# Kernel tuning notes

Hardware: AMD Instinct MI355X
Metric: run time of the kernel (lower is better)

Reference implementation:

```python
import jax, jax.numpy as jnp
import numpy as np

N_NODES = 50000
N_EDGES = 800000
BATCH = 4


def setup_inputs() -> dict:
    key = jax.random.key(0)
    ks = jax.random.split(key, 12)
    inp = {
        "x": jax.random.normal(ks[0], (BATCH, N_NODES, 1, 1), dtype=jnp.float32),
        "edge_index": jax.random.randint(ks[1], (2, N_EDGES), 0, N_NODES, dtype=jnp.int64),
        "W_conv1": jax.random.normal(ks[2], (3, 1, 32), dtype=jnp.float32) * 0.1,
        "b_conv1": jnp.zeros((3, 32), dtype=jnp.float32),
        "W_lin1": jax.random.normal(ks[3], (3, 64, 32), dtype=jnp.float32) * 0.1,
        "b_lin1": jnp.zeros((3, 32), dtype=jnp.float32),
        "att1": jax.random.uniform(ks[4], (1,), dtype=jnp.float32),
        "W_conv2": jax.random.normal(ks[5], (3, 32, 32), dtype=jnp.float32) * 0.1,
        "b_conv2": jnp.zeros((3, 32), dtype=jnp.float32),
        "W_lin2": jax.random.normal(ks[6], (3, 64, 32), dtype=jnp.float32) * 0.1,
        "b_lin2": jnp.zeros((3, 32), dtype=jnp.float32),
        "att2": jax.random.uniform(ks[7], (1,), dtype=jnp.float32),
        "W_out": jax.random.normal(ks[8], (32, 1), dtype=jnp.float32) * 0.1,
        "b_out": jnp.zeros((1,), dtype=jnp.float32),
    }
    return inp


def _gcn(h, W, b, src, dst, norm, inv_deg, n):
    # h: (B,N,Fin) -> (B,N,Fout); symmetric-normalized GCNConv with self loops
    xw = h @ W                                   # (B,N,Fout)
    msg = xw[:, src, :] * norm[None, :, None]    # (B,E,Fout)
    agg = jax.ops.segment_sum(jnp.swapaxes(msg, 0, 1), dst, num_segments=n)
    agg = jnp.swapaxes(agg, 0, 1)                # (B,N,Fout)
    return agg + xw * inv_deg[None, :, None] + b


def _tgcn_cell(h_in, Wc, bc, Wl, bl, att, src, dst, norm, inv_deg, n):
    # TGCN2 GRU cell with H0 = 0, weighted by softmax(att) (periods=1 -> weight 1)
    B = h_in.shape[0]
    out_dim = Wc.shape[-1]
    H = jnp.zeros((B, n, out_dim), dtype=h_in.dtype)
    cz = _gcn(h_in, Wc[0], bc[0], src, dst, norm, inv_deg, n)
    Z = jax.nn.sigmoid(jnp.concatenate([cz, H], axis=-1) @ Wl[0] + bl[0])
    cr = _gcn(h_in, Wc[1], bc[1], src, dst, norm, inv_deg, n)
    R = jax.nn.sigmoid(jnp.concatenate([cr, H], axis=-1) @ Wl[1] + bl[1])
    ch = _gcn(h_in, Wc[2], bc[2], src, dst, norm, inv_deg, n)
    Ht = jnp.tanh(jnp.concatenate([ch, H * R], axis=-1) @ Wl[2] + bl[2])
    Hn = Z * H + (1.0 - Z) * Ht
    a = jax.nn.softmax(att)  # (1,) -> [1.0]
    return a[0] * Hn


def reference(x, edge_index, W_conv1, b_conv1, W_lin1, b_lin1, att1,
              W_conv2, b_conv2, W_lin2, b_lin2, att2, W_out, b_out):
    n = x.shape[1]
    src, dst = edge_index[0], edge_index[1]
    ones = jnp.ones(src.shape[0], dtype=x.dtype)
    deg = jax.ops.segment_sum(ones, dst, num_segments=n) + 1.0  # + self loop
    dis = jax.lax.rsqrt(deg)
    norm = dis[src] * dis[dst]   # (E,)
    inv_deg = 1.0 / deg          # self-loop norm

    h = x[..., 0]  # (B,N,1) periods=1
    h = jax.nn.relu(_tgcn_cell(h, W_conv1, b_conv1, W_lin1, b_lin1, att1,
                               src, dst, norm, inv_deg, n))
    h = jax.nn.relu(_tgcn_cell(h, W_conv2, b_conv2, W_lin2, b_lin2, att2,
                               src, dst, norm, inv_deg, n))
    return h @ W_out + b_out  # (B,N,1)
```

## Files before the change

kernel.cpp:

```cpp
#include <hip/hip_runtime.h>
#include <hip/hip_fp16.h>
#include <stdint.h>

#define N_NODES 50000
#define BATCH 4
#define CAP 64

__global__ void fill_kernel(const int* __restrict__ src,
                            const int* __restrict__ dst,
                            int* __restrict__ cursor,
                            unsigned short* __restrict__ bucket, int E) {
    int e = blockIdx.x * blockDim.x + threadIdx.x;
    if (e < E) {
        int d = dst[e];
        int pos = atomicAdd(&cursor[d], 1);
        if (pos < CAP) bucket[d * CAP + pos] = (unsigned short)src[e];
    }
}

__global__ void dis_xd_kernel(const int* __restrict__ deg,
                              const float* __restrict__ x,
                              float* __restrict__ dis,
                              float4* __restrict__ xd, int N) {
    int n = blockIdx.x * blockDim.x + threadIdx.x;
    if (n >= N) return;
    float d = rsqrtf((float)(deg[n] + 1));
    dis[n] = d;
    xd[n] = make_float4(x[n] * d, x[N + n] * d, x[2 * N + n] * d,
                        x[3 * N + n] * d);
}

__global__ void precomp_kernel(const float* __restrict__ Wc1,
                               const float* __restrict__ bc1,
                               const float* __restrict__ Wl1,
                               const float* __restrict__ bl1,
                               const float* __restrict__ Wc2,
                               const float* __restrict__ bc2,
                               const float* __restrict__ Wl2,
                               const float* __restrict__ bl2,
                               float* __restrict__ pc) {
    int i = blockIdx.x * blockDim.x + threadIdx.x;
    if (i < 2048) {
        int g = i >> 10;
        int kf = i & 1023;
        int k = kf >> 5, f = kf & 31;
        int gate = g ? 2 : 0;
        float s = 0.0f;
        for (int j = 0; j < 32; ++j)
            s += Wc2[gate * 1024 + k * 32 + j] * Wl2[gate * 2048 + j * 32 + f];
        pc[i] = s;
    } else if (i < 2112) {
        int g = (i - 2048) >> 5;
        int f = i & 31;
        int gate = g ? 2 : 0;
        float s = bl2[gate * 32 + f];
        for (int j = 0; j < 32; ++j)
            s += bc2[gate * 32 + j] * Wl2[gate * 2048 + j * 32 + f];
        pc[i] = s;
    } else if (i < 2240) {
        int t = i - 2112;
        int which = t >> 5;
        int f = t & 31;
        int gate = (which >= 2) ? 2 : 0;
        if ((which & 1) == 0) {
            float s = 0.0f;
            for (int j = 0; j < 32; ++j)
                s += Wc1[gate * 32 + j] * Wl1[gate * 2048 + j * 32 + f];
            pc[i] = s;
        } else {
            float s = bl1[gate * 32 + f];
            for (int j = 0; j < 32; ++j)
                s += bc1[gate * 32 + j] * Wl1[gate * 2048 + j * 32 + f];
            pc[i] = s;
        }
    }
}

__global__ void s1h1_kernel(const float4* __restrict__ xd,
                            const float* __restrict__ dis,
                            const int* __restrict__ deg,
                            const unsigned short* __restrict__ bucket,
                            const float* __restrict__ pc,
                            char* __restrict__ hs, int N) {
    int idx = blockIdx.x * blockDim.x + threadIdx.x;
    int node = idx >> 3;
    if (node >= N) return;
    int j = idx & 7;
    int cnt = deg[node];
    if (cnt > CAP) cnt = CAP;
    float ax, ay, az, aw;
    if (j == 0) {
        float4 v = xd[node];
        ax = v.x; ay = v.y; az = v.z; aw = v.w;
    } else {
        ax = ay = az = aw = 0.f;
    }
    for (int i = j; i < cnt; i += 8) {
        int s = bucket[node * CAP + i];
        float4 v = xd[s];
        ax += v.x; ay += v.y; az += v.z; aw += v.w;
    }
#pragma unroll
    for (int m = 4; m; m >>= 1) {
        ax += __shfl_xor(ax, m, 64);
        ay += __shfl_xor(ay, m, 64);
        az += __shfl_xor(az, m, 64);
        aw += __shfl_xor(aw, m, 64);
    }
    float d = dis[node];
    float t0 = ax * d, t1 = ay * d, t2 = az * d, t3 = aw * d;
#pragma unroll
    for (int m = 0; m < 4; ++m) {
        int f = j + 8 * m;
        float uz = pc[2112 + f], vz = pc[2144 + f];
        float uh = pc[2176 + f], vh = pc[2208 + f];
        float h0 = fmaxf((1.0f - 1.0f / (1.0f + expf(-(t0 * uz + vz)))) *
                         tanhf(t0 * uh + vh), 0.0f) * d;
        float h1 = fmaxf((1.0f - 1.0f / (1.0f + expf(-(t1 * uz + vz)))) *
                         tanhf(t1 * uh + vh), 0.0f) * d;
        float h2 = fmaxf((1.0f - 1.0f / (1.0f + expf(-(t2 * uz + vz)))) *
                         tanhf(t2 * uh + vh), 0.0f) * d;
        float h3 = fmaxf((1.0f - 1.0f / (1.0f + expf(-(t3 * uz + vz)))) *
                         tanhf(t3 * uh + vh), 0.0f) * d;
        __half2 lo = __floats2half2_rn(h0, h1);
        __half2 hi = __floats2half2_rn(h2, h3);
        uint2 u;
        u.x = *reinterpret_cast<unsigned int*>(&lo);
        u.y = *reinterpret_cast<unsigned int*>(&hi);
        *reinterpret_cast<uint2*>(hs + (size_t)node * 256 + f * 8) = u;
    }
}

__global__ __launch_bounds__(256) void l2_agg_kernel(
    const char* __restrict__ hs, const float* __restrict__ dis,
    const int* __restrict__ deg, const unsigned short* __restrict__ bucket,
    const float* __restrict__ pc, const float* __restrict__ Wout,
    const float* __restrict__ bout, float* __restrict__ out, int N) {
    int lane = threadIdx.x & 63;
    int f = lane & 31;
    int h = lane >> 5;

    float mcol[32];
#pragma unroll
    for (int k = 0; k < 32; ++k) mcol[k] = pc[h * 1024 + k * 32 + f];
    float wv = pc[2048 + h * 32 + f];
    float wf = Wout[f];
    float bo = bout[0];
    const char* hp = hs + f * 8 + h * 4;

    int wid = (blockIdx.x * blockDim.x + threadIdx.x) >> 6;
    int nw = (gridDim.x * blockDim.x) >> 6;

    for (int node = wid; node < N; node += nw) {
        int cnt = deg[node];
        if (cnt > CAP) cnt = CAP;
        unsigned int bidx = bucket[node * CAP + lane];
        __half2 sv = *(const __half2*)(hp + (size_t)node * 256);
        float2 fs = __half22float2(sv);
        float accx = fs.x, accy = fs.y;
        int i = 0;
        for (; i + 8 <= cnt; i += 8) {
            unsigned int o0 = __builtin_amdgcn_readlane(bidx, i) * 256u;
            unsigned int o1 = __builtin_amdgcn_readlane(bidx, i + 1) * 256u;
            unsigned int o2 = __builtin_amdgcn_readlane(bidx, i + 2) * 256u;
            unsigned int o3 = __builtin_amdgcn_readlane(bidx, i + 3) * 256u;
            unsigned int o4 = __builtin_amdgcn_readlane(bidx, i + 4) * 256u;
            unsigned int o5 = __builtin_amdgcn_readlane(bidx, i + 5) * 256u;
            unsigned int o6 = __builtin_amdgcn_readlane(bidx, i + 6) * 256u;
            unsigned int o7 = __builtin_amdgcn_readlane(bidx, i + 7) * 256u;
            __half2 v0 = *(const __half2*)(hp + o0);
            __half2 v1 = *(const __half2*)(hp + o1);
            __half2 v2 = *(const __half2*)(hp + o2);
            __half2 v3 = *(const __half2*)(hp + o3);
            __half2 v4 = *(const __half2*)(hp + o4);
            __half2 v5 = *(const __half2*)(hp + o5);
            __half2 v6 = *(const __half2*)(hp + o6);
            __half2 v7 = *(const __half2*)(hp + o7);
            float2 f0 = __half22float2(v0), f1 = __half22float2(v1);
            float2 f2 = __half22float2(v2), f3 = __half22float2(v3);
            float2 f4 = __half22float2(v4), f5 = __half22float2(v5);
            float2 f6 = __half22float2(v6), f7 = __half22float2(v7);
            accx += ((f0.x + f1.x) + (f2.x + f3.x)) +
                    ((f4.x + f5.x) + (f6.x + f7.x));
            accy += ((f0.y + f1.y) + (f2.y + f3.y)) +
                    ((f4.y + f5.y) + (f6.y + f7.y));
        }
        for (; i < cnt; ++i) {
            unsigned int o = __builtin_amdgcn_readlane(bidx, i) * 256u;
            float2 fv = __half22float2(*(const __half2*)(hp + o));
            accx += fv.x;
            accy += fv.y;
        }

        float g0 = 0.f, g1 = 0.f, g2 = 0.f, g3 = 0.f;
#pragma unroll
        for (int k = 0; k < 32; ++k) {
            float tb0 = __int_as_float(
                __builtin_amdgcn_readlane(__float_as_int(accx), k));
            float tb1 = __int_as_float(
                __builtin_amdgcn_readlane(__float_as_int(accy), k));
            float tb2 = __int_as_float(
                __builtin_amdgcn_readlane(__float_as_int(accx), 32 + k));
            float tb3 = __int_as_float(
                __builtin_amdgcn_readlane(__float_as_int(accy), 32 + k));
            float m = mcol[k];
            g0 += tb0 * m; g1 += tb1 * m; g2 += tb2 * m; g3 += tb3 * m;
        }
        float dn = dis[node];
        float a0 = dn * g0 + wv, a1 = dn * g1 + wv;
        float a2 = dn * g2 + wv, a3 = dn * g3 + wv;
        float v0 = h ? tanhf(a0) : 1.0f / (1.0f + expf(-a0));
        float v1 = h ? tanhf(a1) : 1.0f / (1.0f + expf(-a1));
        float v2 = h ? tanhf(a2) : 1.0f / (1.0f + expf(-a2));
        float v3 = h ? tanhf(a3) : 1.0f / (1.0f + expf(-a3));
        float p0 = __shfl_xor(v0, 32, 64);
        float p1 = __shfl_xor(v1, 32, 64);
        float p2 = __shfl_xor(v2, 32, 64);
        float p3 = __shfl_xor(v3, 32, 64);
        if (h == 0) {
            float o0 = fmaxf((1.0f - v0) * p0, 0.0f) * wf;
            float o1 = fmaxf((1.0f - v1) * p1, 0.0f) * wf;
            float o2 = fmaxf((1.0f - v2) * p2, 0.0f) * wf;
            float o3 = fmaxf((1.0f - v3) * p3, 0.0f) * wf;
#pragma unroll
            for (int d = 16; d; d >>= 1) {
                o0 += __shfl_xor(o0, d, 64);
                o1 += __shfl_xor(o1, d, 64);
                o2 += __shfl_xor(o2, d, 64);
                o3 += __shfl_xor(o3, d, 64);
            }
            if (f == 0) {
                out[node] = o0 + bo;
                out[(size_t)N + node] = o1 + bo;
                out[(size_t)2 * N + node] = o2 + bo;
                out[(size_t)3 * N + node] = o3 + bo;
            }
        }
    }
}


extern "C" void kernel_launch(void* const* d_in, const int* in_sizes, int n_in,
                              void* d_out, int out_size, void* d_ws,
                              size_t ws_size, hipStream_t stream) {
    const float* x    = (const float*)d_in[0];
    const int*   ei   = (const int*)d_in[1];
    const float* Wc1  = (const float*)d_in[2];
    const float* bc1  = (const float*)d_in[3];
    const float* Wl1  = (const float*)d_in[4];
    const float* bl1  = (const float*)d_in[5];
    const float* Wc2  = (const float*)d_in[7];
    const float* bc2  = (const float*)d_in[8];
    const float* Wl2  = (const float*)d_in[9];
    const float* bl2  = (const float*)d_in[10];
    const float* Wout = (const float*)d_in[12];
    const float* bout = (const float*)d_in[13];

    const int E = in_sizes[1] / 2;
    const int N = N_NODES;
    const int* src = ei;
    const int* dst = ei + E;

    char* p = (char*)d_ws;
    auto alloc = [&](size_t bytes) {
        char* r = p;
        p += (bytes + 15) & ~(size_t)15;
        return r;
    };
    int*            cursor = (int*)alloc(N * sizeof(int));
    unsigned short* bucket = (unsigned short*)alloc((size_t)N * CAP * 2);
    float*          dis    = (float*)alloc(N * sizeof(float));
    float*          xd     = (float*)alloc((size_t)N * 4 * sizeof(float));
    char*           hs     = (char*)alloc((size_t)N * 256);
    float*          pc     = (float*)alloc(2240 * sizeof(float));

    hipMemsetAsync(cursor, 0, N * sizeof(int), stream);

    precomp_kernel<<<(2240 + 255) / 256, 256, 0, stream>>>(
        Wc1, bc1, Wl1, bl1, Wc2, bc2, Wl2, bl2, pc);

    fill_kernel<<<(E + 255) / 256, 256, 0, stream>>>(src, dst, cursor, bucket,
                                                     E);
    dis_xd_kernel<<<(N + 255) / 256, 256, 0, stream>>>(cursor, x, dis,
                                                       (float4*)xd, N);

    s1h1_kernel<<<(N * 8 + 255) / 256, 256, 0, stream>>>(
        (const float4*)xd, dis, cursor, bucket, pc, hs, N);

    l2_agg_kernel<<<2048, 256, 0, stream>>>(hs, dis, cursor, bucket, pc, Wout,
                                            bout, (float*)d_out, N);
}
```

Measured before the change: 218.0 us.

## Fuse all stages into one persistent kernel with grid barriers

Replaces the memset and five separate kernel launches with a single persistent kernel of 1024 blocks. The stages are separated by a software grid-wide barrier built on agent-scope atomics. The layer-2 neighbor accumulation now sums in half2 arithmetic instead of converting each value to float. The sigmoid is rewritten as 0.5*tanh(x/2)+0.5 so that both gate lanes follow a uniform tanh path. These changes aim to remove launch overhead and some conversion and divergence work, at the cost of reduced accumulation precision and a barrier that depends on all 1024 blocks being resident at the same time.

```diff
diff --git a/kernel.cpp b/kernel.cpp
--- a/kernel.cpp
+++ b/kernel.cpp
@@ -3,237 +3,248 @@
 #include <stdint.h>
 
 #define N_NODES 50000
-#define BATCH 4
 #define CAP 64
-
-__global__ void fill_kernel(const int* __restrict__ src,
-                            const int* __restrict__ dst,
-                            int* __restrict__ cursor,
-                            unsigned short* __restrict__ bucket, int E) {
-    int e = blockIdx.x * blockDim.x + threadIdx.x;
-    if (e < E) {
+#define NBLK 1024
+#define NTHR 256
+#define TOTAL (NBLK * NTHR)
+
+__device__ __forceinline__ void gsync(int* bar, int phase) {
+    __syncthreads();
+    if (threadIdx.x == 0) {
+        __threadfence();
+        int old = __hip_atomic_fetch_add(&bar[0], 1, __ATOMIC_ACQ_REL,
+                                         __HIP_MEMORY_SCOPE_AGENT);
+        if (old == NBLK - 1) {
+            __hip_atomic_store(&bar[0], 0, __ATOMIC_RELAXED,
+                               __HIP_MEMORY_SCOPE_AGENT);
+            __hip_atomic_store(&bar[1], phase, __ATOMIC_RELEASE,
+                               __HIP_MEMORY_SCOPE_AGENT);
+        } else {
+            while (__hip_atomic_load(&bar[1], __ATOMIC_ACQUIRE,
+                                     __HIP_MEMORY_SCOPE_AGENT) < phase)
+                __builtin_amdgcn_s_sleep(2);
+        }
+    }
+    __syncthreads();
+}
+
+__global__ __launch_bounds__(NTHR, 8) void mega_kernel(
+    const float* __restrict__ x, const int* __restrict__ src,
+    const int* __restrict__ dst, const float* __restrict__ Wc1,
+    const float* __restrict__ bc1, const float* __restrict__ Wl1,
+    const float* __restrict__ bl1, const float* __restrict__ Wc2,
+    const float* __restrict__ bc2, const float* __restrict__ Wl2,
+    const float* __restrict__ bl2, const float* __restrict__ Wout,
+    const float* __restrict__ bout, float* __restrict__ out,
+    int* __restrict__ cursor, unsigned short* __restrict__ bucket,
+    float* __restrict__ dis, float4* __restrict__ xd, char* __restrict__ hs,
+    float* __restrict__ pc, int* bar, int E, int N) {
+    const int tid = blockIdx.x * NTHR + threadIdx.x;
+
+    if (tid < N) cursor[tid] = 0;
+    if (tid < 2240) {
+        int i = tid;
+        if (i < 2048) {
+            int g = i >> 10;
+            int kf = i & 1023;
+            int k = kf >> 5, f = kf & 31;
+            int gate = g ? 2 : 0;
+            float s = 0.0f;
+            for (int j = 0; j < 32; ++j)
+                s += Wc2[gate * 1024 + k * 32 + j] *
+                     Wl2[gate * 2048 + j * 32 + f];
+            pc[i] = s;
+        } else if (i < 2112) {
+            int g = (i - 2048) >> 5;
+            int f = i & 31;
+            int gate = g ? 2 : 0;
+            float s = bl2[gate * 32 + f];
+            for (int j = 0; j < 32; ++j)
+                s += bc2[gate * 32 + j] * Wl2[gate * 2048 + j * 32 + f];
+            pc[i] = s;
+        } else {
+            int t = i - 2112;
+            int which = t >> 5;
+            int f = t & 31;
+            int gate = (which >= 2) ? 2 : 0;
+            if ((which & 1) == 0) {
+                float s = 0.0f;
+                for (int j = 0; j < 32; ++j)
+                    s += Wc1[gate * 32 + j] * Wl1[gate * 2048 + j * 32 + f];
+                pc[i] = s;
+            } else {
+                float s = bl1[gate * 32 + f];
+                for (int j = 0; j < 32; ++j)
+                    s += bc1[gate * 32 + j] * Wl1[gate * 2048 + j * 32 + f];
+                pc[i] = s;
+            }
+        }
+    }
+    gsync(bar, 1);
+
+    for (int e = tid; e < E; e += TOTAL) {
         int d = dst[e];
         int pos = atomicAdd(&cursor[d], 1);
         if (pos < CAP) bucket[d * CAP + pos] = (unsigned short)src[e];
     }
-}
-
-__global__ void dis_xd_kernel(const int* __restrict__ deg,
-                              const float* __restrict__ x,
-                              float* __restrict__ dis,
-                              float4* __restrict__ xd, int N) {
-    int n = blockIdx.x * blockDim.x + threadIdx.x;
-    if (n >= N) return;
-    float d = rsqrtf((float)(deg[n] + 1));
-    dis[n] = d;
-    xd[n] = make_float4(x[n] * d, x[N + n] * d, x[2 * N + n] * d,
-                        x[3 * N + n] * d);
-}
-
-__global__ void precomp_kernel(const float* __restrict__ Wc1,
-                               const float* __restrict__ bc1,
-                               const float* __restrict__ Wl1,
-                               const float* __restrict__ bl1,
-                               const float* __restrict__ Wc2,
-                               const float* __restrict__ bc2,
-                               const float* __restrict__ Wl2,
-                               const float* __restrict__ bl2,
-                               float* __restrict__ pc) {
-    int i = blockIdx.x * blockDim.x + threadIdx.x;
-    if (i < 2048) {
-        int g = i >> 10;
-        int kf = i & 1023;
-        int k = kf >> 5, f = kf & 31;
-        int gate = g ? 2 : 0;
-        float s = 0.0f;
-        for (int j = 0; j < 32; ++j)
-            s += Wc2[gate * 1024 + k * 32 + j] * Wl2[gate * 2048 + j * 32 + f];
-        pc[i] = s;
-    } else if (i < 2112) {
-        int g = (i - 2048) >> 5;
-        int f = i & 31;
-        int gate = g ? 2 : 0;
-        float s = bl2[gate * 32 + f];
-        for (int j = 0; j < 32; ++j)
-            s += bc2[gate * 32 + j] * Wl2[gate * 2048 + j * 32 + f];
-        pc[i] = s;
-    } else if (i < 2240) {
-        int t = i - 2112;
-        int which = t >> 5;
-        int f = t & 31;
-        int gate = (which >= 2) ? 2 : 0;
-        if ((which & 1) == 0) {
-            float s = 0.0f;
-            for (int j = 0; j < 32; ++j)
-                s += Wc1[gate * 32 + j] * Wl1[gate * 2048 + j * 32 + f];
-            pc[i] = s;
+    gsync(bar, 2);
+
+    if (tid < N) {
+        float d = rsqrtf((float)(cursor[tid] + 1));
+        dis[tid] = d;
+        xd[tid] = make_float4(x[tid] * d, x[N + tid] * d, x[2 * N + tid] * d,
+                              x[3 * N + tid] * d);
+    }
+    gsync(bar, 3);
+
+    for (int idx = tid; idx < N * 8; idx += TOTAL) {
+        int node = idx >> 3;
+        int j = idx & 7;
+        int cnt = cursor[node];
+        if (cnt > CAP) cnt = CAP;
+        float ax, ay, az, aw;
+        if (j == 0) {
+            float4 v = xd[node];
+            ax = v.x; ay = v.y; az = v.z; aw = v.w;
         } else {
-            float s = bl1[gate * 32 + f];
-            for (int j = 0; j < 32; ++j)
-                s += bc1[gate * 32 + j] * Wl1[gate * 2048 + j * 32 + f];
-            pc[i] = s;
-        }
-    }
-}
-
-__global__ void s1h1_kernel(const float4* __restrict__ xd,
-                            const float* __restrict__ dis,
-                            const int* __restrict__ deg,
-                            const unsigned short* __restrict__ bucket,
-                            const float* __restrict__ pc,
-                            char* __restrict__ hs, int N) {
-    int idx = blockIdx.x * blockDim.x + threadIdx.x;
-    int node = idx >> 3;
-    if (node >= N) return;
-    int j = idx & 7;
-    int cnt = deg[node];
-    if (cnt > CAP) cnt = CAP;
-    float ax, ay, az, aw;
-    if (j == 0) {
-        float4 v = xd[node];
-        ax = v.x; ay = v.y; az = v.z; aw = v.w;
-    } else {
-        ax = ay = az = aw = 0.f;
-    }
-    for (int i = j; i < cnt; i += 8) {
-        int s = bucket[node * CAP + i];
-        float4 v = xd[s];
-        ax += v.x; ay += v.y; az += v.z; aw += v.w;
-    }
-#pragma unroll
-    for (int m = 4; m; m >>= 1) {
-        ax += __shfl_xor(ax, m, 64);
-        ay += __shfl_xor(ay, m, 64);
-        az += __shfl_xor(az, m, 64);
-        aw += __shfl_xor(aw, m, 64);
-    }
-    float d = dis[node];
-    float t0 = ax * d, t1 = ay * d, t2 = az * d, t3 = aw * d;
-#pragma unroll
-    for (int m = 0; m < 4; ++m) {
-        int f = j + 8 * m;
-        float uz = pc[2112 + f], vz = pc[2144 + f];
-        float uh = pc[2176 + f], vh = pc[2208 + f];
-        float h0 = fmaxf((1.0f - 1.0f / (1.0f + expf(-(t0 * uz + vz)))) *
-                         tanhf(t0 * uh + vh), 0.0f) * d;
-        float h1 = fmaxf((1.0f - 1.0f / (1.0f + expf(-(t1 * uz + vz)))) *
-                         tanhf(t1 * uh + vh), 0.0f) * d;
-        float h2 = fmaxf((1.0f - 1.0f / (1.0f + expf(-(t2 * uz + vz)))) *
-                         tanhf(t2 * uh + vh), 0.0f) * d;
-        float h3 = fmaxf((1.0f - 1.0f / (1.0f + expf(-(t3 * uz + vz)))) *
-                         tanhf(t3 * uh + vh), 0.0f) * d;
-        __half2 lo = __floats2half2_rn(h0, h1);
-        __half2 hi = __floats2half2_rn(h2, h3);
-        uint2 u;
-        u.x = *reinterpret_cast<unsigned int*>(&lo);
-        u.y = *reinterpret_cast<unsigned int*>(&hi);
-        *reinterpret_cast<uint2*>(hs + (size_t)node * 256 + f * 8) = u;
-    }
-}
-
-__global__ __launch_bounds__(256) void l2_agg_kernel(
-    const char* __restrict__ hs, const float* __restrict__ dis,
-    const int* __restrict__ deg, const unsigned short* __restrict__ bucket,
-    const float* __restrict__ pc, const float* __restrict__ Wout,
-    const float* __restrict__ bout, float* __restrict__ out, int N) {
-    int lane = threadIdx.x & 63;
-    int f = lane & 31;
-    int h = lane >> 5;
-
-    float mcol[32];
-#pragma unroll
-    for (int k = 0; k < 32; ++k) mcol[k] = pc[h * 1024 + k * 32 + f];
-    float wv = pc[2048 + h * 32 + f];
-    float wf = Wout[f];
-    float bo = bout[0];
-    const char* hp = hs + f * 8 + h * 4;
-
-    int wid = (blockIdx.x * blockDim.x + threadIdx.x) >> 6;
-    int nw = (gridDim.x * blockDim.x) >> 6;
-
-    for (int node = wid; node < N; node += nw) {
-        int cnt = deg[node];
-        if (cnt > CAP) cnt = CAP;
-        unsigned int bidx = bucket[node * CAP + lane];
-        __half2 sv = *(const __half2*)(hp + (size_t)node * 256);
-        float2 fs = __half22float2(sv);
-        float accx = fs.x, accy = fs.y;
-        int i = 0;
-        for (; i + 8 <= cnt; i += 8) {
-            unsigned int o0 = __builtin_amdgcn_readlane(bidx, i) * 256u;
-            unsigned int o1 = __builtin_amdgcn_readlane(bidx, i + 1) * 256u;
-            unsigned int o2 = __builtin_amdgcn_readlane(bidx, i + 2) * 256u;
-            unsigned int o3 = __builtin_amdgcn_readlane(bidx, i + 3) * 256u;
-            unsigned int o4 = __builtin_amdgcn_readlane(bidx, i + 4) * 256u;
-            unsigned int o5 = __builtin_amdgcn_readlane(bidx, i + 5) * 256u;
-            unsigned int o6 = __builtin_amdgcn_readlane(bidx, i + 6) * 256u;
-            unsigned int o7 = __builtin_amdgcn_readlane(bidx, i + 7) * 256u;
-            __half2 v0 = *(const __half2*)(hp + o0);
-            __half2 v1 = *(const __half2*)(hp + o1);
-            __half2 v2 = *(const __half2*)(hp + o2);
-            __half2 v3 = *(const __half2*)(hp + o3);
-            __half2 v4 = *(const __half2*)(hp + o4);
-            __half2 v5 = *(const __half2*)(hp + o5);
-            __half2 v6 = *(const __half2*)(hp + o6);
-            __half2 v7 = *(const __half2*)(hp + o7);
-            float2 f0 = __half22float2(v0), f1 = __half22float2(v1);
-            float2 f2 = __half22float2(v2), f3 = __half22float2(v3);
-            float2 f4 = __half22float2(v4), f5 = __half22float2(v5);
-            float2 f6 = __half22float2(v6), f7 = __half22float2(v7);
-            accx += ((f0.x + f1.x) + (f2.x + f3.x)) +
-                    ((f4.x + f5.x) + (f6.x + f7.x));
-            accy += ((f0.y + f1.y) + (f2.y + f3.y)) +
-                    ((f4.y + f5.y) + (f6.y + f7.y));
-        }
-        for (; i < cnt; ++i) {
-            unsigned int o = __builtin_amdgcn_readlane(bidx, i) * 256u;
-            float2 fv = __half22float2(*(const __half2*)(hp + o));
-            accx += fv.x;
-            accy += fv.y;
-        }
-
-        float g0 = 0.f, g1 = 0.f, g2 = 0.f, g3 = 0.f;
-#pragma unroll
-        for (int k = 0; k < 32; ++k) {
-            float tb0 = __int_as_float(
-                __builtin_amdgcn_readlane(__float_as_int(accx), k));
-            float tb1 = __int_as_float(
-                __builtin_amdgcn_readlane(__float_as_int(accy), k));
-            float tb2 = __int_as_float(
-                __builtin_amdgcn_readlane(__float_as_int(accx), 32 + k));
-            float tb3 = __int_as_float(
-                __builtin_amdgcn_readlane(__float_as_int(accy), 32 + k));
-            float m = mcol[k];
-            g0 += tb0 * m; g1 += tb1 * m; g2 += tb2 * m; g3 += tb3 * m;
-        }
-        float dn = dis[node];
-        float a0 = dn * g0 + wv, a1 = dn * g1 + wv;
-        float a2 = dn * g2 + wv, a3 = dn * g3 + wv;
-        float v0 = h ? tanhf(a0) : 1.0f / (1.0f + expf(-a0));
-        float v1 = h ? tanhf(a1) : 1.0f / (1.0f + expf(-a1));
-        float v2 = h ? tanhf(a2) : 1.0f / (1.0f + expf(-a2));
-        float v3 = h ? tanhf(a3) : 1.0f / (1.0f + expf(-a3));
-        float p0 = __shfl_xor(v0, 32, 64);
-        float p1 = __shfl_xor(v1, 32, 64);
-        float p2 = __shfl_xor(v2, 32, 64);
-        float p3 = __shfl_xor(v3, 32, 64);
-        if (h == 0) {
-            float o0 = fmaxf((1.0f - v0) * p0, 0.0f) * wf;
-            float o1 = fmaxf((1.0f - v1) * p1, 0.0f) * wf;
-            float o2 = fmaxf((1.0f - v2) * p2, 0.0f) * wf;
-            float o3 = fmaxf((1.0f - v3) * p3, 0.0f) * wf;
-#pragma unroll
-            for (int d = 16; d; d >>= 1) {
-                o0 += __shfl_xor(o0, d, 64);
-                o1 += __shfl_xor(o1, d, 64);
-                o2 += __shfl_xor(o2, d, 64);
-                o3 += __shfl_xor(o3, d, 64);
-            }
-            if (f == 0) {
-                out[node] = o0 + bo;
-                out[(size_t)N + node] = o1 + bo;
-                out[(size_t)2 * N + node] = o2 + bo;
-                out[(size_t)3 * N + node] = o3 + bo;
+            ax = ay = az = aw = 0.f;
+        }
+        for (int i = j; i < cnt; i += 8) {
+            int s = bucket[node * CAP + i];
+            float4 v = xd[s];
+            ax += v.x; ay += v.y; az += v.z; aw += v.w;
+        }
+#pragma unroll
+        for (int m = 4; m; m >>= 1) {
+            ax += __shfl_xor(ax, m, 64);
+            ay += __shfl_xor(ay, m, 64);
+            az += __shfl_xor(az, m, 64);
+            aw += __shfl_xor(aw, m, 64);
+        }
+        float d = dis[node];
+        float t0 = ax * d, t1 = ay * d, t2 = az * d, t3 = aw * d;
+#pragma unroll
+        for (int m = 0; m < 4; ++m) {
+            int f = j + 8 * m;
+            float uz = pc[2112 + f], vz = pc[2144 + f];
+            float uh = pc[2176 + f], vh = pc[2208 + f];
+            float h0 = fmaxf((1.0f - 1.0f / (1.0f + expf(-(t0 * uz + vz)))) *
+                             tanhf(t0 * uh + vh), 0.0f) * d;
+            float h1 = fmaxf((1.0f - 1.0f / (1.0f + expf(-(t1 * uz + vz)))) *
+                             tanhf(t1 * uh + vh), 0.0f) * d;
+            float h2 = fmaxf((1.0f - 1.0f / (1.0f + expf(-(t2 * uz + vz)))) *
+                             tanhf(t2 * uh + vh), 0.0f) * d;
+            float h3 = fmaxf((1.0f - 1.0f / (1.0f + expf(-(t3 * uz + vz)))) *
+                             tanhf(t3 * uh + vh), 0.0f) * d;
+            __half2 lo = __floats2half2_rn(h0, h1);
+            __half2 hi = __floats2half2_rn(h2, h3);
+            uint2 u;
+            u.x = *reinterpret_cast<unsigned int*>(&lo);
+            u.y = *reinterpret_cast<unsigned int*>(&hi);
+            *reinterpret_cast<uint2*>(hs + (size_t)node * 256 + f * 8) = u;
+        }
+    }
+    gsync(bar, 4);
+
+    {
+        int lane = threadIdx.x & 63;
+        int f = lane & 31;
+        int h = lane >> 5;
+        float mcol[32];
+#pragma unroll
+        for (int k = 0; k < 32; ++k) mcol[k] = pc[h * 1024 + k * 32 + f];
+        float wv = pc[2048 + h * 32 + f];
+        float wf = Wout[f];
+        float bo = bout[0];
+        const char* hp = hs + f * 8 + h * 4;
+
+        int wid = tid >> 6;
+        int nw = TOTAL >> 6;
+
+        for (int node = wid; node < N; node += nw) {
+            int cnt = cursor[node];
+            if (cnt > CAP) cnt = CAP;
+            unsigned int bidx = bucket[node * CAP + lane];
+            __half2 acc = *(const __half2*)(hp + (size_t)node * 256);
+            int i = 0;
+            for (; i + 8 <= cnt; i += 8) {
+                unsigned int o0 = __builtin_amdgcn_readlane(bidx, i) * 256u;
+                unsigned int o1 = __builtin_amdgcn_readlane(bidx, i + 1) * 256u;
+                unsigned int o2 = __builtin_amdgcn_readlane(bidx, i + 2) * 256u;
+                unsigned int o3 = __builtin_amdgcn_readlane(bidx, i + 3) * 256u;
+                unsigned int o4 = __builtin_amdgcn_readlane(bidx, i + 4) * 256u;
+                unsigned int o5 = __builtin_amdgcn_readlane(bidx, i + 5) * 256u;
+                unsigned int o6 = __builtin_amdgcn_readlane(bidx, i + 6) * 256u;
+                unsigned int o7 = __builtin_amdgcn_readlane(bidx, i + 7) * 256u;
+                __half2 v0 = *(const __half2*)(hp + o0);
+                __half2 v1 = *(const __half2*)(hp + o1);
+                __half2 v2 = *(const __half2*)(hp + o2);
+                __half2 v3 = *(const __half2*)(hp + o3);
+                __half2 v4 = *(const __half2*)(hp + o4);
+                __half2 v5 = *(const __half2*)(hp + o5);
+                __half2 v6 = *(const __half2*)(hp + o6);
+                __half2 v7 = *(const __half2*)(hp + o7);
+                __half2 s01 = __hadd2(v0, v1);
+                __half2 s23 = __hadd2(v2, v3);
+                __half2 s45 = __hadd2(v4, v5);
+                __half2 s67 = __hadd2(v6, v7);
+                __half2 s03 = __hadd2(s01, s23);
+                __half2 s47 = __hadd2(s45, s67);
+                acc = __hadd2(acc, __hadd2(s03, s47));
+            }
+            for (; i < cnt; ++i) {
+                unsigned int o = __builtin_amdgcn_readlane(bidx, i) * 256u;
+                acc = __hadd2(acc, *(const __half2*)(hp + o));
+            }
+            float2 fa = __half22float2(acc);
+            float accx = fa.x, accy = fa.y;
+
+            float g0 = 0.f, g1 = 0.f, g2 = 0.f, g3 = 0.f;
+#pragma unroll
+            for (int k = 0; k < 32; ++k) {
+                float tb0 = __int_as_float(
+                    __builtin_amdgcn_readlane(__float_as_int(accx), k));
+                float tb1 = __int_as_float(
+                    __builtin_amdgcn_readlane(__float_as_int(accy), k));
+                float tb2 = __int_as_float(
+                    __builtin_amdgcn_readlane(__float_as_int(accx), 32 + k));
+                float tb3 = __int_as_float(
+                    __builtin_amdgcn_readlane(__float_as_int(accy), 32 + k));
+                float m = mcol[k];
+                g0 += tb0 * m; g1 += tb1 * m; g2 += tb2 * m; g3 += tb3 * m;
+            }
+            float dn = dis[node];
+            float a0 = dn * g0 + wv, a1 = dn * g1 + wv;
+            float a2 = dn * g2 + wv, a3 = dn * g3 + wv;
+            float sc = h ? 1.0f : 0.5f;
+            float q0 = tanhf(a0 * sc), q1 = tanhf(a1 * sc);
+            float q2 = tanhf(a2 * sc), q3 = tanhf(a3 * sc);
+            float v0 = h ? q0 : fmaf(0.5f, q0, 0.5f);
+            float v1 = h ? q1 : fmaf(0.5f, q1, 0.5f);
+            float v2 = h ? q2 : fmaf(0.5f, q2, 0.5f);
+            float v3 = h ? q3 : fmaf(0.5f, q3, 0.5f);
+            float p0 = __shfl_xor(v0, 32, 64);
+            float p1 = __shfl_xor(v1, 32, 64);
+            float p2 = __shfl_xor(v2, 32, 64);
+            float p3 = __shfl_xor(v3, 32, 64);
+            if (h == 0) {
+                float o0 = fmaxf((1.0f - v0) * p0, 0.0f) * wf;
+                float o1 = fmaxf((1.0f - v1) * p1, 0.0f) * wf;
+                float o2 = fmaxf((1.0f - v2) * p2, 0.0f) * wf;
+                float o3 = fmaxf((1.0f - v3) * p3, 0.0f) * wf;
+#pragma unroll
+                for (int d = 16; d; d >>= 1) {
+                    o0 += __shfl_xor(o0, d, 64);
+                    o1 += __shfl_xor(o1, d, 64);
+                    o2 += __shfl_xor(o2, d, 64);
+                    o3 += __shfl_xor(o3, d, 64);
+                }
+                if (f == 0) {
+                    out[node] = o0 + bo;
+                    out[(size_t)N + node] = o1 + bo;
+                    out[(size_t)2 * N + node] = o2 + bo;
+                    out[(size_t)3 * N + node] = o3 + bo;
+                }
             }
         }
     }
@@ -267,6 +278,7 @@
         p += (bytes + 15) & ~(size_t)15;
         return r;
     };
+    int*            bar    = (int*)alloc(4 * sizeof(int));
     int*            cursor = (int*)alloc(N * sizeof(int));
     unsigned short* bucket = (unsigned short*)alloc((size_t)N * CAP * 2);
     float*          dis    = (float*)alloc(N * sizeof(float));
@@ -274,19 +286,9 @@
     char*           hs     = (char*)alloc((size_t)N * 256);
     float*          pc     = (float*)alloc(2240 * sizeof(float));
 
-    hipMemsetAsync(cursor, 0, N * sizeof(int), stream);
-
-    precomp_kernel<<<(2240 + 255) / 256, 256, 0, stream>>>(
-        Wc1, bc1, Wl1, bl1, Wc2, bc2, Wl2, bl2, pc);
-
-    fill_kernel<<<(E + 255) / 256, 256, 0, stream>>>(src, dst, cursor, bucket,
-                                                     E);
-    dis_xd_kernel<<<(N + 255) / 256, 256, 0, stream>>>(cursor, x, dis,
-                                                       (float4*)xd, N);
-
-    s1h1_kernel<<<(N * 8 + 255) / 256, 256, 0, stream>>>(
-        (const float4*)xd, dis, cursor, bucket, pc, hs, N);
-
-    l2_agg_kernel<<<2048, 256, 0, stream>>>(hs, dis, cursor, bucket, pc, Wout,
-                                            bout, (float*)d_out, N);
+    hipMemsetAsync(bar, 0, 4 * sizeof(int), stream);
+
+    mega_kernel<<<NBLK, NTHR, 0, stream>>>(
+        x, src, dst, Wc1, bc1, Wl1, bl1, Wc2, bc2, Wl2, bl2, Wout, bout,
+        (float*)d_out, cursor, bucket, dis, (float4*)xd, hs, pc, bar, E, N);
 }
```

New measurement: 814.0 us. +273.3%, slower.

## Fuse memset into precompute kernel, accumulate in half2, transpose gate matmul via LDS

Applied to the files above, without the earlier changes.

The cursor memset is folded into the weight-precompute kernel, which removes one launch. The neighbour gather now accumulates in half2 instead of converting each value to float. The per-node 32x32 gate matmul no longer uses 128 readlanes; each wave writes its aggregate to LDS and every lane computes both the z and h gates for two batch entries with vectorized LDS reads. The cost is more registers (two 32-wide weight columns per lane) and lower precision from summing up to 64 neighbours in fp16.

```diff
diff --git a/kernel.cpp b/kernel.cpp
--- a/kernel.cpp
+++ b/kernel.cpp
@@ -6,40 +6,19 @@
 #define BATCH 4
 #define CAP 64
 
-__global__ void fill_kernel(const int* __restrict__ src,
-                            const int* __restrict__ dst,
-                            int* __restrict__ cursor,
-                            unsigned short* __restrict__ bucket, int E) {
-    int e = blockIdx.x * blockDim.x + threadIdx.x;
-    if (e < E) {
-        int d = dst[e];
-        int pos = atomicAdd(&cursor[d], 1);
-        if (pos < CAP) bucket[d * CAP + pos] = (unsigned short)src[e];
-    }
-}
-
-__global__ void dis_xd_kernel(const int* __restrict__ deg,
-                              const float* __restrict__ x,
-                              float* __restrict__ dis,
-                              float4* __restrict__ xd, int N) {
-    int n = blockIdx.x * blockDim.x + threadIdx.x;
-    if (n >= N) return;
-    float d = rsqrtf((float)(deg[n] + 1));
-    dis[n] = d;
-    xd[n] = make_float4(x[n] * d, x[N + n] * d, x[2 * N + n] * d,
-                        x[3 * N + n] * d);
-}
-
-__global__ void precomp_kernel(const float* __restrict__ Wc1,
-                               const float* __restrict__ bc1,
-                               const float* __restrict__ Wl1,
-                               const float* __restrict__ bl1,
-                               const float* __restrict__ Wc2,
-                               const float* __restrict__ bc2,
-                               const float* __restrict__ Wl2,
-                               const float* __restrict__ bl2,
-                               float* __restrict__ pc) {
+__global__ void zero_precomp_kernel(int* __restrict__ cursor,
+                                    const float* __restrict__ Wc1,
+                                    const float* __restrict__ bc1,
+                                    const float* __restrict__ Wl1,
+                                    const float* __restrict__ bl1,
+                                    const float* __restrict__ Wc2,
+                                    const float* __restrict__ bc2,
+                                    const float* __restrict__ Wl2,
+                                    const float* __restrict__ bl2,
+                                    float* __restrict__ pc, int N) {
     int i = blockIdx.x * blockDim.x + threadIdx.x;
+    if (i < N) cursor[i] = 0;
+    if (i >= 2240) return;
     if (i < 2048) {
         int g = i >> 10;
         int kf = i & 1023;
@@ -57,7 +36,7 @@
         for (int j = 0; j < 32; ++j)
             s += bc2[gate * 32 + j] * Wl2[gate * 2048 + j * 32 + f];
         pc[i] = s;
-    } else if (i < 2240) {
+    } else {
         int t = i - 2112;
         int which = t >> 5;
         int f = t & 31;
@@ -74,6 +53,30 @@
             pc[i] = s;
         }
     }
+}
+
+__global__ void fill_kernel(const int* __restrict__ src,
+                            const int* __restrict__ dst,
+                            int* __restrict__ cursor,
+                            unsigned short* __restrict__ bucket, int E) {
+    int e = blockIdx.x * blockDim.x + threadIdx.x;
+    if (e < E) {
+        int d = dst[e];
+        int pos = atomicAdd(&cursor[d], 1);
+        if (pos < CAP) bucket[d * CAP + pos] = (unsigned short)src[e];
+    }
+}
+
+__global__ void dis_xd_kernel(const int* __restrict__ deg,
+                              const float* __restrict__ x,
+                              float* __restrict__ dis,
+                              float4* __restrict__ xd, int N) {
+    int n = blockIdx.x * blockDim.x + threadIdx.x;
+    if (n >= N) return;
+    float d = rsqrtf((float)(deg[n] + 1));
+    dis[n] = d;
+    xd[n] = make_float4(x[n] * d, x[N + n] * d, x[2 * N + n] * d,
+                        x[3 * N + n] * d);
 }
 
 __global__ void s1h1_kernel(const float4* __restrict__ xd,
@@ -136,14 +139,19 @@
     const int* __restrict__ deg, const unsigned short* __restrict__ bucket,
     const float* __restrict__ pc, const float* __restrict__ Wout,
     const float* __restrict__ bout, float* __restrict__ out, int N) {
+    __shared__ float2 sT[4][64];
+    int wv = threadIdx.x >> 6;
     int lane = threadIdx.x & 63;
     int f = lane & 31;
     int h = lane >> 5;
 
-    float mcol[32];
-#pragma unroll
-    for (int k = 0; k < 32; ++k) mcol[k] = pc[h * 1024 + k * 32 + f];
-    float wv = pc[2048 + h * 32 + f];
+    float wl0[32], wl2[32];
+#pragma unroll
+    for (int k = 0; k < 32; ++k) {
+        wl0[k] = pc[k * 32 + f];
+        wl2[k] = pc[1024 + k * 32 + f];
+    }
+    float w0 = pc[2048 + f], w2 = pc[2080 + f];
     float wf = Wout[f];
     float bo = bout[0];
     const char* hp = hs + f * 8 + h * 4;
@@ -155,9 +163,7 @@
         int cnt = deg[node];
         if (cnt > CAP) cnt = CAP;
         unsigned int bidx = bucket[node * CAP + lane];
-        __half2 sv = *(const __half2*)(hp + (size_t)node * 256);
-        float2 fs = __half22float2(sv);
-        float accx = fs.x, accy = fs.y;
+        __half2 acc = *(const __half2*)(hp + (size_t)node * 256);
         int i = 0;
         for (; i + 8 <= cnt; i += 8) {
             unsigned int o0 = __builtin_amdgcn_readlane(bidx, i) * 256u;
@@ -176,65 +182,48 @@
             __half2 v5 = *(const __half2*)(hp + o5);
             __half2 v6 = *(const __half2*)(hp + o6);
             __half2 v7 = *(const __half2*)(hp + o7);
-            float2 f0 = __half22float2(v0), f1 = __half22float2(v1);
-            float2 f2 = __half22float2(v2), f3 = __half22float2(v3);
-            float2 f4 = __half22float2(v4), f5 = __half22float2(v5);
-            float2 f6 = __half22float2(v6), f7 = __half22float2(v7);
-            accx += ((f0.x + f1.x) + (f2.x + f3.x)) +
-                    ((f4.x + f5.x) + (f6.x + f7.x));
-            accy += ((f0.y + f1.y) + (f2.y + f3.y)) +
-                    ((f4.y + f5.y) + (f6.y + f7.y));
+            __half2 s01 = __hadd2(v0, v1);
+            __half2 s23 = __hadd2(v2, v3);
+            __half2 s45 = __hadd2(v4, v5);
+            __half2 s67 = __hadd2(v6, v7);
+            acc = __hadd2(acc, __hadd2(__hadd2(s01, s23), __hadd2(s45, s67)));
         }
         for (; i < cnt; ++i) {
             unsigned int o = __builtin_amdgcn_readlane(bidx, i) * 256u;
-            float2 fv = __half22float2(*(const __half2*)(hp + o));
-            accx += fv.x;
-            accy += fv.y;
-        }
-
-        float g0 = 0.f, g1 = 0.f, g2 = 0.f, g3 = 0.f;
-#pragma unroll
-        for (int k = 0; k < 32; ++k) {
-            float tb0 = __int_as_float(
-                __builtin_amdgcn_readlane(__float_as_int(accx), k));
-            float tb1 = __int_as_float(
-                __builtin_amdgcn_readlane(__float_as_int(accy), k));
-            float tb2 = __int_as_float(
-                __builtin_amdgcn_readlane(__float_as_int(accx), 32 + k));
-            float tb3 = __int_as_float(
-                __builtin_amdgcn_readlane(__float_as_int(accy), 32 + k));
-            float m = mcol[k];
-            g0 += tb0 * m; g1 += tb1 * m; g2 += tb2 * m; g3 += tb3 * m;
+            acc = __hadd2(acc, *(const __half2*)(hp + o));
+        }
+        float2 fa = __half22float2(acc);
+
+        sT[wv][lane] = fa;
+
+        float sz0 = 0.f, sz1 = 0.f, sh0 = 0.f, sh1 = 0.f;
+        const float2* tp = &sT[wv][h * 32];
+#pragma unroll
+        for (int k = 0; k < 32; k += 2) {
+            float4 t2 = *(const float4*)&tp[k];
+            sz0 += t2.x * wl0[k];     sz1 += t2.y * wl0[k];
+            sh0 += t2.x * wl2[k];     sh1 += t2.y * wl2[k];
+            sz0 += t2.z * wl0[k + 1]; sz1 += t2.w * wl0[k + 1];
+            sh0 += t2.z * wl2[k + 1]; sh1 += t2.w * wl2[k + 1];
         }
         float dn = dis[node];
-        float a0 = dn * g0 + wv, a1 = dn * g1 + wv;
-        float a2 = dn * g2 + wv, a3 = dn * g3 + wv;
-        float v0 = h ? tanhf(a0) : 1.0f / (1.0f + expf(-a0));
-        float v1 = h ? tanhf(a1) : 1.0f / (1.0f + expf(-a1));
-        float v2 = h ? tanhf(a2) : 1.0f / (1.0f + expf(-a2));
-        float v3 = h ? tanhf(a3) : 1.0f / (1.0f + expf(-a3));
-        float p0 = __shfl_xor(v0, 32, 64);
-        float p1 = __shfl_xor(v1, 32, 64);
-        float p2 = __shfl_xor(v2, 32, 64);
-        float p3 = __shfl_xor(v3, 32, 64);
-        if (h == 0) {
-            float o0 = fmaxf((1.0f - v0) * p0, 0.0f) * wf;
-            float o1 = fmaxf((1.0f - v1) * p1, 0.0f) * wf;
-            float o2 = fmaxf((1.0f - v2) * p2, 0.0f) * wf;
-            float o3 = fmaxf((1.0f - v3) * p3, 0.0f) * wf;
-#pragma unroll
-            for (int d = 16; d; d >>= 1) {
-                o0 += __shfl_xor(o0, d, 64);
-                o1 += __shfl_xor(o1, d, 64);
-                o2 += __shfl_xor(o2, d, 64);
-                o3 += __shfl_xor(o3, d, 64);
-            }
-            if (f == 0) {
-                out[node] = o0 + bo;
-                out[(size_t)N + node] = o1 + bo;
-                out[(size_t)2 * N + node] = o2 + bo;
-                out[(size_t)3 * N + node] = o3 + bo;
-            }
+        float z0 = 1.0f / (1.0f + expf(-(dn * sz0 + w0)));
+        float z1 = 1.0f / (1.0f + expf(-(dn * sz1 + w0)));
+        float t0 = tanhf(dn * sh0 + w2);
+        float t1 = tanhf(dn * sh1 + w2);
+        float h20 = fmaxf((1.0f - z0) * t0, 0.0f);
+        float h21 = fmaxf((1.0f - z1) * t1, 0.0f);
+
+        float o0 = h20 * wf;
+        float o1 = h21 * wf;
+#pragma unroll
+        for (int d = 16; d; d >>= 1) {
+            o0 += __shfl_xor(o0, d, 64);
+            o1 += __shfl_xor(o1, d, 64);
+        }
+        if (f == 0) {
+            out[(size_t)(2 * h) * N + node] = o0 + bo;
+            out[(size_t)(2 * h + 1) * N + node] = o1 + bo;
         }
     }
 }
@@ -274,16 +263,13 @@
     char*           hs     = (char*)alloc((size_t)N * 256);
     float*          pc     = (float*)alloc(2240 * sizeof(float));
 
-    hipMemsetAsync(cursor, 0, N * sizeof(int), stream);
-
-    precomp_kernel<<<(2240 + 255) / 256, 256, 0, stream>>>(
-        Wc1, bc1, Wl1, bl1, Wc2, bc2, Wl2, bl2, pc);
+    zero_precomp_kernel<<<(N + 255) / 256, 256, 0, stream>>>(
+        cursor, Wc1, bc1, Wl1, bl1, Wc2, bc2, Wl2, bl2, pc, N);
 
     fill_kernel<<<(E + 255) / 256, 256, 0, stream>>>(src, dst, cursor, bucket,
                                                      E);
     dis_xd_kernel<<<(N + 255) / 256, 256, 0, stream>>>(cursor, x, dis,
                                                        (float4*)xd, N);
-
     s1h1_kernel<<<(N * 8 + 255) / 256, 256, 0, stream>>>(
         (const float4*)xd, dis, cursor, bucket, pc, hs, N);
 
```

Measured after the change: 219.1 us. No clear change (+0.5%).
